# Performance work log

Measured on AMD Instinct MI355X. Metric: run time of the kernel, lower is better.

## Reference

```python
import jax, jax.numpy as jnp
import numpy as np
import math

EMBED = 256
HEADS = 4
HEAD_DIM = EMBED // HEADS
OUT_DIM = 256
LN_EPS = 1e-5


def _qkv_init(key):
    # diagonal-domination init from Galerkin Transformer (Cao): U(-spread,spread)*gain + delta*I
    spread = math.sqrt(3.0 / EMBED)
    gain, delta = 0.01, 0.01
    w = jax.random.uniform(key, (EMBED, EMBED), minval=-spread, maxval=spread) * gain
    return w + delta * jnp.eye(EMBED, dtype=w.dtype)


def setup_inputs() -> dict:
    key = jax.random.key(0)
    ks = jax.random.split(key, 6)
    seq = jax.random.normal(ks[0], (4, 8192, EMBED), dtype=jnp.float32)
    wq = _qkv_init(ks[1])
    wk = _qkv_init(ks[2])
    wv = _qkv_init(ks[3])
    # nn.Linear default init for wo
    bound = 1.0 / math.sqrt(EMBED)
    wo = jax.random.uniform(ks[4], (OUT_DIM, EMBED), minval=-bound, maxval=bound)
    bo = jax.random.uniform(ks[5], (OUT_DIM,), minval=-bound, maxval=bound)
    ln_k_g = jnp.ones((HEAD_DIM,), jnp.float32)
    ln_k_b = jnp.zeros((HEAD_DIM,), jnp.float32)
    ln_v_g = jnp.ones((HEAD_DIM,), jnp.float32)
    ln_v_b = jnp.zeros((HEAD_DIM,), jnp.float32)
    return {"seq": seq, "wq": wq, "wk": wk, "wv": wv, "wo": wo, "bo": bo,
            "ln_k_g": ln_k_g, "ln_k_b": ln_k_b, "ln_v_g": ln_v_g, "ln_v_b": ln_v_b}


def _layer_norm(x, g, b):
    mu = jnp.mean(x, axis=-1, keepdims=True)
    var = jnp.mean(jnp.square(x - mu), axis=-1, keepdims=True)
    return (x - mu) * jax.lax.rsqrt(var + LN_EPS) * g + b


def _split_heads(x, B, S):
    # [B, S, E] -> [B, H, S, D]
    return x.reshape(B, S, HEADS, HEAD_DIM).transpose(0, 2, 1, 3)


def reference(seq, wq, wk, wv, wo, bo, ln_k_g, ln_k_b, ln_v_g, ln_v_b):
    B, S, _ = seq.shape
    q = _split_heads(seq @ wq.T, B, S)
    k = _split_heads(seq @ wk.T, B, S)
    v = _split_heads(seq @ wv.T, B, S)
    k = _layer_norm(k, ln_k_g, ln_k_b)
    v = _layer_norm(v, ln_v_g, ln_v_b)
    # Galerkin (softmax-free) attention: Q @ (K^T V) / n  -- O(n d^2)
    kv = jnp.einsum('bhsd,bhse->bhde', k, v) / S   # [B,H,D,D]
    ga = jnp.einsum('bhsd,bhde->bhse', q, kv)       # [B,H,S,D]
    ga = ga.transpose(0, 2, 1, 3).reshape(B, S, EMBED)
    return ga @ wo.T + bo
```

## Files before the change

### kernel.cpp

```cpp
#include <hip/hip_runtime.h>
#include <hip/hip_bf16.h>
#include <stdint.h>


#define EMBED 256
#define SEQ   8192
#define LN_EPS 1e-5f

using bf16x8 = __attribute__((ext_vector_type(8))) short;
using bf16x4 = __attribute__((ext_vector_type(4))) short;
using f32x4  = __attribute__((ext_vector_type(4))) float;

static __device__ __forceinline__ short f2bf(float f) {
  __hip_bfloat16 h = __float2bfloat16(f);
  return __builtin_bit_cast(short, h);
}
static __device__ __forceinline__ float bf2f(uint32_t u) {
  return __uint_as_float(u << 16);
}

#define MFMA16(a, b, c) __builtin_amdgcn_mfma_f32_16x16x32_bf16((a), (b), (c), 0, 0, 0)

template <int ROWS>
static __device__ __forceinline__ void stage_x(char* smem, const float* __restrict__ src, int tid) {
#pragma unroll
  for (int i = 0; i < ROWS / 8; ++i) {
    int g = tid + i * 256;
    int row = g >> 5, c16 = g & 31;
    const f32x4* p = (const f32x4*)(src + row * EMBED + c16 * 8);
    f32x4 f0 = p[0], f1 = p[1];
    bf16x8 v;
    v[0] = f2bf(f0[0]); v[1] = f2bf(f0[1]); v[2] = f2bf(f0[2]); v[3] = f2bf(f0[3]);
    v[4] = f2bf(f1[0]); v[5] = f2bf(f1[1]); v[6] = f2bf(f1[2]); v[7] = f2bf(f1[3]);
    *(bf16x8*)(smem + row * 512 + ((c16 * 16) ^ ((row & 7) << 4))) = v;
  }
}

__global__ void gka_prep(const float* __restrict__ wq, const float* __restrict__ wk,
                         const float* __restrict__ wv,
                         unsigned short* __restrict__ wkf, unsigned short* __restrict__ wvf,
                         unsigned short* __restrict__ wqt) {
  __shared__ unsigned short T[64 * 66];
  int blk = blockIdx.x, tid = threadIdx.x;
  if (blk < 64) {
    int g = (blk & 31) * 256 + tid;
    const float* W = (blk < 32) ? wk : wv;
    unsigned short* D = (blk < 32) ? wkf : wvf;
    int wid = g >> 11, kk = (g >> 8) & 7, n = (g >> 6) & 3, ln = g & 63;
    int row = wid * 64 + n * 16 + (ln & 15);
    int c0 = kk * 32 + (ln >> 4) * 8;
    const f32x4* p = (const f32x4*)(W + row * 256 + c0);
    f32x4 f0 = p[0], f1 = p[1];
    bf16x8 v;
    v[0] = f2bf(f0[0]); v[1] = f2bf(f0[1]); v[2] = f2bf(f0[2]); v[3] = f2bf(f0[3]);
    v[4] = f2bf(f1[0]); v[5] = f2bf(f1[1]); v[6] = f2bf(f1[2]); v[7] = f2bf(f1[3]);
    *(bf16x8*)(D + g * 8) = v;
    return;
  }
  int t = blk - 64, ti = t >> 2, tj = t & 3;
#pragma unroll
  for (int it = 0; it < 4; ++it) {
    int g = tid + it * 256;
    int jl = g >> 4, g4 = g & 15;
    f32x4 f = *(const f32x4*)(wq + (tj * 64 + jl) * 256 + ti * 64 + g4 * 4);
#pragma unroll
    for (int q = 0; q < 4; ++q) T[jl * 66 + g4 * 4 + q] = (unsigned short)f2bf(f[q]);
  }
  __syncthreads();
#pragma unroll
  for (int it = 0; it < 2; ++it) {
    int g = tid + it * 256;
    int il = g >> 3, j8 = g & 7;
    bf16x8 v;
#pragma unroll
    for (int q = 0; q < 8; ++q) v[q] = (short)T[(j8 * 8 + q) * 66 + il];
    *(bf16x8*)(wqt + (ti * 64 + il) * 256 + tj * 64 + j8 * 8) = v;
  }
}

__global__ __launch_bounds__(256, 2)
void gka_kv(const float* __restrict__ seq,
            const unsigned short* __restrict__ wkf, const unsigned short* __restrict__ wvf,
            const float* __restrict__ lkg, const float* __restrict__ lkb,
            const float* __restrict__ lvg, const float* __restrict__ lvb,
            unsigned short* __restrict__ P) {
  __shared__ char smem[65536];
  const int tid = threadIdx.x;
  const int lane = tid & 63;
  const int wid = tid >> 6;
  const int l15 = lane & 15, l4 = lane >> 4, l7 = lane & 7;
  const int tile = blockIdx.x;
  const int b = tile >> 7;
  const int ptile = tile & 127;

  stage_x<64>(smem, seq + (size_t)(b * SEQ + ptile * 64) * EMBED, tid);
  __syncthreads();

  f32x4 acck[4][4], accv[4][4];
#pragma unroll
  for (int m = 0; m < 4; ++m)
#pragma unroll
    for (int n = 0; n < 4; ++n) { acck[m][n] = (f32x4)0.0f; accv[m][n] = (f32x4)0.0f; }

#pragma unroll
  for (int kk = 0; kk < 8; ++kk) {
    bf16x8 af[4], bwk[4], bwv[4];
#pragma unroll
    for (int m = 0; m < 4; ++m) {
      int row = m * 16 + l15;
      af[m] = *(const bf16x8*)(smem + row * 512 + ((kk * 64 + l4 * 16) ^ (l7 << 4)));
    }
#pragma unroll
    for (int n = 0; n < 4; ++n) {
      size_t off = (((wid * 8 + kk) * 4 + n) * 64 + lane) << 3;
      bwk[n] = *(const bf16x8*)(wkf + off);
      bwv[n] = *(const bf16x8*)(wvf + off);
    }
#pragma unroll
    for (int m = 0; m < 4; ++m)
#pragma unroll
      for (int n = 0; n < 4; ++n) {
        acck[m][n] = MFMA16(af[m], bwk[n], acck[m][n]);
        accv[m][n] = MFMA16(af[m], bwv[n], accv[m][n]);
      }
  }

  __syncthreads();

#pragma unroll
  for (int mat = 0; mat < 2; ++mat) {
    const f32x4 (*acc)[4] = mat ? accv : acck;
    const float* gp = mat ? lvg : lkg;
    const float* bp = mat ? lvb : lkb;
    float gv[4], bv[4];
#pragma unroll
    for (int n = 0; n < 4; ++n) { gv[n] = gp[n * 16 + l15]; bv[n] = bp[n * 16 + l15]; }
    char* T = smem + (mat ? 0 : 32768) + wid * 8192;
#pragma unroll
    for (int m = 0; m < 4; ++m) {
      float mu[4], rs[4];
#pragma unroll
      for (int r = 0; r < 4; ++r) {
        float s1 = 0.f, s2 = 0.f;
#pragma unroll
        for (int n = 0; n < 4; ++n) { float x = acc[m][n][r]; s1 += x; s2 += x * x; }
#pragma unroll
        for (int msk = 1; msk < 16; msk <<= 1) {
          s1 += __shfl_xor(s1, msk);
          s2 += __shfl_xor(s2, msk);
        }
        mu[r] = s1 * (1.f / 64.f);
        float var = s2 * (1.f / 64.f) - mu[r] * mu[r];
        rs[r] = rsqrtf(var + LN_EPS);
      }
#pragma unroll
      for (int n = 0; n < 4; ++n) {
        bf16x4 pk;
#pragma unroll
        for (int r = 0; r < 4; ++r)
          pk[r] = f2bf((acc[m][n][r] - mu[r]) * rs[r] * gv[n] + bv[n]);
        int d = n * 16 + l15;
        int sb = m * 32 + l4 * 8;
        *(bf16x4*)(T + d * 128 + (sb ^ (l7 << 4))) = pk;
      }
    }
  }

  __syncthreads();

  f32x4 a2[4][4];
#pragma unroll
  for (int fd = 0; fd < 4; ++fd)
#pragma unroll
    for (int n = 0; n < 4; ++n) a2[fd][n] = (f32x4)0.0f;

#pragma unroll
  for (int kk = 0; kk < 2; ++kk) {
    bf16x8 ak[4], bv2[4];
#pragma unroll
    for (int fd = 0; fd < 4; ++fd) {
      int d = fd * 16 + l15;
      ak[fd] = *(const bf16x8*)(smem + 32768 + wid * 8192 + d * 128 +
                                ((kk * 64 + l4 * 16) ^ (l7 << 4)));
    }
#pragma unroll
    for (int n = 0; n < 4; ++n) {
      int e = n * 16 + l15;
      bv2[n] = *(const bf16x8*)(smem + wid * 8192 + e * 128 +
                                ((kk * 64 + l4 * 16) ^ (l7 << 4)));
    }
#pragma unroll
    for (int fd = 0; fd < 4; ++fd)
#pragma unroll
      for (int n = 0; n < 4; ++n)
        a2[fd][n] = MFMA16(ak[fd], bv2[n], a2[fd][n]);
  }

  unsigned short* Ph = P + ((size_t)((b * 128 + ptile) * 4 + wid) << 12);
#pragma unroll
  for (int fd = 0; fd < 4; ++fd)
#pragma unroll
    for (int n = 0; n < 4; ++n) {
      bf16x4 pk;
#pragma unroll
      for (int r = 0; r < 4; ++r) pk[r] = f2bf(a2[fd][n][r]);
      *(bf16x4*)(Ph + (fd * 4 + n) * 256 + lane * 4) = pk;
    }
}

__global__ __launch_bounds__(256)
void gka_red(const unsigned short* __restrict__ P, float* __restrict__ kvf) {
  int gtid = blockIdx.x * 256 + threadIdx.x;
  int chunk = gtid & 7;
  int qid = gtid >> 3;
  int b = qid >> 12, h = (qid >> 10) & 3, t4 = qid & 1023;
  const unsigned short* p0 = P + ((size_t)(b * 512 + h) << 12) + t4 * 4;
  float s0 = 0.f, s1 = 0.f, s2 = 0.f, s3 = 0.f;
#pragma unroll
  for (int s = 0; s < 16; ++s) {
    int p = chunk * 16 + s;
    uint2 u = *(const uint2*)(p0 + ((size_t)p << 14));
    s0 += bf2f(u.x & 0xffffu); s1 += bf2f(u.x >> 16);
    s2 += bf2f(u.y & 0xffffu); s3 += bf2f(u.y >> 16);
  }
#pragma unroll
  for (int msk = 1; msk < 8; msk <<= 1) {
    s0 += __shfl_xor(s0, msk); s1 += __shfl_xor(s1, msk);
    s2 += __shfl_xor(s2, msk); s3 += __shfl_xor(s3, msk);
  }
  if (chunk == 0) {
    f32x4 r; r[0] = s0; r[1] = s1; r[2] = s2; r[3] = s3;
    *(f32x4*)(kvf + (qid << 2)) = r;
  }
}

__global__ __launch_bounds__(256, 2)
void gka_m1(const float* __restrict__ kvf, const float* __restrict__ wo,
            unsigned short* __restrict__ m1t) {
  const int tid = threadIdx.x;
  const int lane = tid & 63;
  const int wid = tid >> 6;
  const int l15 = lane & 15, l4 = lane >> 4;
  const int blk = blockIdx.x;
  const int b = blk >> 2, h = blk & 3;
  const float invS = 1.f / (float)SEQ;
  const float* kvh = kvf + ((b * 4 + h) << 12);

  f32x4 acc[4][4];
#pragma unroll
  for (int m = 0; m < 4; ++m)
#pragma unroll
    for (int n = 0; n < 4; ++n) acc[m][n] = (f32x4)0.0f;

#pragma unroll
  for (int kk = 0; kk < 2; ++kk) {
    bf16x8 af[4], bw[4];
#pragma unroll
    for (int m = 0; m < 4; ++m) {
      int base = (m * 4 + kk * 2 + (l4 >> 1)) * 256 +
                 ((l15 >> 2) * 16 + (l4 & 1) * 8) * 4 + (l15 & 3);
      bf16x8 v;
#pragma unroll
      for (int j = 0; j < 8; ++j) v[j] = f2bf(kvh[base + j * 4] * invS);
      af[m] = v;
    }
#pragma unroll
    for (int n = 0; n < 4; ++n) {
      int o = wid * 64 + n * 16 + l15;
      const f32x4* wp = (const f32x4*)(wo + (size_t)o * 256 + h * 64 + kk * 32 + l4 * 8);
      f32x4 w0 = wp[0], w1 = wp[1];
      bf16x8 v;
      v[0] = f2bf(w0[0]); v[1] = f2bf(w0[1]); v[2] = f2bf(w0[2]); v[3] = f2bf(w0[3]);
      v[4] = f2bf(w1[0]); v[5] = f2bf(w1[1]); v[6] = f2bf(w1[2]); v[7] = f2bf(w1[3]);
      bw[n] = v;
    }
#pragma unroll
    for (int m = 0; m < 4; ++m)
#pragma unroll
      for (int n = 0; n < 4; ++n)
        acc[m][n] = MFMA16(af[m], bw[n], acc[m][n]);
  }
#pragma unroll
  for (int m = 0; m < 4; ++m)
#pragma unroll
    for (int n = 0; n < 4; ++n) {
      int o = wid * 64 + n * 16 + l15;
      int j0 = h * 64 + m * 16 + l4 * 4;
      bf16x4 pk;
#pragma unroll
      for (int r = 0; r < 4; ++r) pk[r] = f2bf(acc[m][n][r]);
      *(bf16x4*)(m1t + (size_t)(b * 256 + o) * 256 + j0) = pk;
    }
}

__global__ __launch_bounds__(512, 2)
void gka_wc(const unsigned short* __restrict__ wqt, const unsigned short* __restrict__ m1t,
            unsigned short* __restrict__ wcf) {
  const int tid = threadIdx.x;
  const int lane = tid & 63;
  const int wid = tid >> 6;
  const int wm = wid >> 2, wn = wid & 3;
  const int l15 = lane & 15, l4 = lane >> 4;
  const int blk = blockIdx.x;
  const int b = blk >> 1, ih = blk & 1;

  f32x4 acc[4][4];
#pragma unroll
  for (int m = 0; m < 4; ++m)
#pragma unroll
    for (int n = 0; n < 4; ++n) acc[m][n] = (f32x4)0.0f;

#pragma unroll
  for (int kk = 0; kk < 8; ++kk) {
    bf16x8 af[4], bw[4];
#pragma unroll
    for (int m = 0; m < 4; ++m) {
      int i = ih * 128 + wm * 64 + m * 16 + l15;
      af[m] = *(const bf16x8*)(wqt + i * 256 + kk * 32 + l4 * 8);
    }
#pragma unroll
    for (int n = 0; n < 4; ++n) {
      int o = wn * 64 + n * 16 + l15;
      bw[n] = *(const bf16x8*)(m1t + (size_t)(b * 256 + o) * 256 + kk * 32 + l4 * 8);
    }
#pragma unroll
    for (int m = 0; m < 4; ++m)
#pragma unroll
      for (int n = 0; n < 4; ++n)
        acc[m][n] = MFMA16(af[m], bw[n], acc[m][n]);
  }
#pragma unroll
  for (int m = 0; m < 4; ++m)
#pragma unroll
    for (int n = 0; n < 4; ++n) {
      int kko = ih * 4 + wm * 2 + (m >> 1);
      int laneo = ((m & 1) * 2 + (l4 >> 1)) * 16 + l15;
      int jo = (l4 & 1) * 4;
      bf16x4 pk;
#pragma unroll
      for (int r = 0; r < 4; ++r) pk[r] = f2bf(acc[m][n][r]);
      *(bf16x4*)(wcf + ((size_t)b << 16) +
                 (((((wn * 8 + kko) * 4 + n) * 64) + laneo) << 3) + jo) = pk;
    }
}

__global__ __launch_bounds__(256, 4)
void gka_out(const float* __restrict__ seq, const unsigned short* __restrict__ wcf,
             const float* __restrict__ bo, float* __restrict__ out) {
  __shared__ char smem[16384];
  const int tid = threadIdx.x;
  const int lane = tid & 63;
  const int wid = tid >> 6;
  const int l15 = lane & 15, l4 = lane >> 4, l7 = lane & 7;
  const int tile = blockIdx.x;
  const int b = tile >> 8;
  const int srow = (tile & 255) * 32;

  stage_x<32>(smem, seq + (size_t)(b * SEQ + srow) * EMBED, tid);

  const unsigned short* Wf = wcf + ((size_t)b << 16);
  float bov[4];
#pragma unroll
  for (int n = 0; n < 4; ++n) bov[n] = bo[wid * 64 + n * 16 + l15];

  f32x4 acc[2][4];
#pragma unroll
  for (int m = 0; m < 2; ++m)
#pragma unroll
    for (int n = 0; n < 4; ++n) acc[m][n] = (f32x4)0.0f;

  __syncthreads();

#pragma unroll
  for (int kk = 0; kk < 8; ++kk) {
    bf16x8 af[2], bw[4];
#pragma unroll
    for (int m = 0; m < 2; ++m) {
      int row = m * 16 + l15;
      af[m] = *(const bf16x8*)(smem + row * 512 + ((kk * 64 + l4 * 16) ^ (l7 << 4)));
    }
#pragma unroll
    for (int n = 0; n < 4; ++n)
      bw[n] = *(const bf16x8*)(Wf + ((((wid * 8 + kk) * 4 + n) * 64 + lane) << 3));
#pragma unroll
    for (int m = 0; m < 2; ++m)
#pragma unroll
      for (int n = 0; n < 4; ++n)
        acc[m][n] = MFMA16(af[m], bw[n], acc[m][n]);
  }

  float* dst = out + (size_t)(b * SEQ + srow) * EMBED;
#pragma unroll
  for (int m = 0; m < 2; ++m)
#pragma unroll
    for (int n = 0; n < 4; ++n)
#pragma unroll
      for (int r = 0; r < 4; ++r)
        dst[(size_t)(m * 16 + l4 * 4 + r) * EMBED + wid * 64 + n * 16 + l15] =
            acc[m][n][r] + bov[n];
}

extern "C" void kernel_launch(void* const* d_in, const int* in_sizes, int n_in,
                              void* d_out, int out_size, void* d_ws, size_t ws_size,
                              hipStream_t stream) {
  const float* seq = (const float*)d_in[0];
  const float* wq  = (const float*)d_in[1];
  const float* wk  = (const float*)d_in[2];
  const float* wv  = (const float*)d_in[3];
  const float* wo  = (const float*)d_in[4];
  const float* bo  = (const float*)d_in[5];
  const float* lkg = (const float*)d_in[6];
  const float* lkb = (const float*)d_in[7];
  const float* lvg = (const float*)d_in[8];
  const float* lvb = (const float*)d_in[9];
  float* out = (float*)d_out;
  char* ws = (char*)d_ws;

  unsigned short* wkf = (unsigned short*)(ws + 0);
  unsigned short* wvf = (unsigned short*)(ws + 131072);
  unsigned short* wqt = (unsigned short*)(ws + 262144);
  float*          kvf = (float*)(ws + 524288);
  unsigned short* m1t = (unsigned short*)(ws + 786432);
  unsigned short* wcf = (unsigned short*)(ws + 1310720);
  unsigned short* P   = (unsigned short*)d_out;

  gka_prep<<<80, 256, 0, stream>>>(wq, wk, wv, wkf, wvf, wqt);
  gka_kv<<<512, 256, 0, stream>>>(seq, wkf, wvf, lkg, lkb, lvg, lvb, P);
  gka_red<<<512, 256, 0, stream>>>(P, kvf);
  gka_m1<<<16, 256, 0, stream>>>(kvf, wo, m1t);
  gka_wc<<<8, 512, 0, stream>>>(wqt, m1t, wcf);
  gka_out<<<1024, 256, 0, stream>>>(seq, wcf, bo, out);
}
```

Baseline: 73.50 us.

## Fuse m1 and wc kernels, staging M1 in swizzled shared memory

Merges the kernel computing M1 = (kv/S)·Wo into the kernel computing the combined weight Wc. Each block now computes a half of M1 for one batch into 64KB of XOR-swizzled LDS, synchronises, then multiplies Wq^T by it. This removes one kernel launch and the global round trip of m1t. In exchange only 8 blocks do all of the m1 work, versus 16 blocks before, and 64KB of LDS per block limits occupancy.

```diff
diff --git a/kernel.cpp b/kernel.cpp
--- a/kernel.cpp
+++ b/kernel.cpp
@@ -234,114 +234,113 @@
   }
 }
 
-__global__ __launch_bounds__(256, 2)
-void gka_m1(const float* __restrict__ kvf, const float* __restrict__ wo,
-            unsigned short* __restrict__ m1t) {
+__global__ __launch_bounds__(512)
+void gka_wc(const float* __restrict__ kvf, const float* __restrict__ wo,
+            const unsigned short* __restrict__ wqt, unsigned short* __restrict__ wcf) {
+  __shared__ char M1[65536];
   const int tid = threadIdx.x;
   const int lane = tid & 63;
   const int wid = tid >> 6;
   const int l15 = lane & 15, l4 = lane >> 4;
   const int blk = blockIdx.x;
-  const int b = blk >> 2, h = blk & 3;
+  const int b = blk >> 1, oh = blk & 1;
   const float invS = 1.f / (float)SEQ;
-  const float* kvh = kvf + ((b * 4 + h) << 12);
-
-  f32x4 acc[4][4];
-#pragma unroll
-  for (int m = 0; m < 4; ++m)
-#pragma unroll
-    for (int n = 0; n < 4; ++n) acc[m][n] = (f32x4)0.0f;
-
-#pragma unroll
-  for (int kk = 0; kk < 2; ++kk) {
-    bf16x8 af[4], bw[4];
-#pragma unroll
-    for (int m = 0; m < 4; ++m) {
-      int base = (m * 4 + kk * 2 + (l4 >> 1)) * 256 +
-                 ((l15 >> 2) * 16 + (l4 & 1) * 8) * 4 + (l15 & 3);
-      bf16x8 v;
-#pragma unroll
-      for (int j = 0; j < 8; ++j) v[j] = f2bf(kvh[base + j * 4] * invS);
-      af[m] = v;
-    }
-#pragma unroll
-    for (int n = 0; n < 4; ++n) {
-      int o = wid * 64 + n * 16 + l15;
-      const f32x4* wp = (const f32x4*)(wo + (size_t)o * 256 + h * 64 + kk * 32 + l4 * 8);
-      f32x4 w0 = wp[0], w1 = wp[1];
-      bf16x8 v;
-      v[0] = f2bf(w0[0]); v[1] = f2bf(w0[1]); v[2] = f2bf(w0[2]); v[3] = f2bf(w0[3]);
-      v[4] = f2bf(w1[0]); v[5] = f2bf(w1[1]); v[6] = f2bf(w1[2]); v[7] = f2bf(w1[3]);
-      bw[n] = v;
-    }
+
+  {
+    const int wo_t = wid >> 2, wj = wid & 3;
+    const float* kvh = kvf + ((b * 4 + wj) << 12);
+    f32x4 acc[4][4];
 #pragma unroll
     for (int m = 0; m < 4; ++m)
 #pragma unroll
-      for (int n = 0; n < 4; ++n)
-        acc[m][n] = MFMA16(af[m], bw[n], acc[m][n]);
-  }
-#pragma unroll
-  for (int m = 0; m < 4; ++m)
-#pragma unroll
-    for (int n = 0; n < 4; ++n) {
-      int o = wid * 64 + n * 16 + l15;
-      int j0 = h * 64 + m * 16 + l4 * 4;
-      bf16x4 pk;
-#pragma unroll
-      for (int r = 0; r < 4; ++r) pk[r] = f2bf(acc[m][n][r]);
-      *(bf16x4*)(m1t + (size_t)(b * 256 + o) * 256 + j0) = pk;
-    }
-}
-
-__global__ __launch_bounds__(512, 2)
-void gka_wc(const unsigned short* __restrict__ wqt, const unsigned short* __restrict__ m1t,
-            unsigned short* __restrict__ wcf) {
-  const int tid = threadIdx.x;
-  const int lane = tid & 63;
-  const int wid = tid >> 6;
-  const int wm = wid >> 2, wn = wid & 3;
-  const int l15 = lane & 15, l4 = lane >> 4;
-  const int blk = blockIdx.x;
-  const int b = blk >> 1, ih = blk & 1;
-
-  f32x4 acc[4][4];
-#pragma unroll
-  for (int m = 0; m < 4; ++m)
-#pragma unroll
-    for (int n = 0; n < 4; ++n) acc[m][n] = (f32x4)0.0f;
-
-#pragma unroll
-  for (int kk = 0; kk < 8; ++kk) {
-    bf16x8 af[4], bw[4];
-#pragma unroll
-    for (int m = 0; m < 4; ++m) {
-      int i = ih * 128 + wm * 64 + m * 16 + l15;
-      af[m] = *(const bf16x8*)(wqt + i * 256 + kk * 32 + l4 * 8);
-    }
-#pragma unroll
-    for (int n = 0; n < 4; ++n) {
-      int o = wn * 64 + n * 16 + l15;
-      bw[n] = *(const bf16x8*)(m1t + (size_t)(b * 256 + o) * 256 + kk * 32 + l4 * 8);
+      for (int n = 0; n < 4; ++n) acc[m][n] = (f32x4)0.0f;
+
+#pragma unroll
+    for (int kk = 0; kk < 2; ++kk) {
+      bf16x8 af[4], bw[4];
+#pragma unroll
+      for (int m = 0; m < 4; ++m) {
+        int base = (m * 4 + kk * 2 + (l4 >> 1)) * 256 +
+                   ((l15 >> 2) * 16 + (l4 & 1) * 8) * 4 + (l15 & 3);
+        bf16x8 v;
+#pragma unroll
+        for (int j = 0; j < 8; ++j) v[j] = f2bf(kvh[base + j * 4] * invS);
+        af[m] = v;
+      }
+#pragma unroll
+      for (int n = 0; n < 4; ++n) {
+        int o = oh * 128 + wo_t * 64 + n * 16 + l15;
+        const f32x4* wp = (const f32x4*)(wo + (size_t)o * 256 + wj * 64 + kk * 32 + l4 * 8);
+        f32x4 w0 = wp[0], w1 = wp[1];
+        bf16x8 v;
+        v[0] = f2bf(w0[0]); v[1] = f2bf(w0[1]); v[2] = f2bf(w0[2]); v[3] = f2bf(w0[3]);
+        v[4] = f2bf(w1[0]); v[5] = f2bf(w1[1]); v[6] = f2bf(w1[2]); v[7] = f2bf(w1[3]);
+        bw[n] = v;
+      }
+#pragma unroll
+      for (int m = 0; m < 4; ++m)
+#pragma unroll
+        for (int n = 0; n < 4; ++n)
+          acc[m][n] = MFMA16(af[m], bw[n], acc[m][n]);
     }
 #pragma unroll
     for (int m = 0; m < 4; ++m)
 #pragma unroll
-      for (int n = 0; n < 4; ++n)
-        acc[m][n] = MFMA16(af[m], bw[n], acc[m][n]);
-  }
-#pragma unroll
-  for (int m = 0; m < 4; ++m)
-#pragma unroll
-    for (int n = 0; n < 4; ++n) {
-      int kko = ih * 4 + wm * 2 + (m >> 1);
-      int laneo = ((m & 1) * 2 + (l4 >> 1)) * 16 + l15;
-      int jo = (l4 & 1) * 4;
-      bf16x4 pk;
-#pragma unroll
-      for (int r = 0; r < 4; ++r) pk[r] = f2bf(acc[m][n][r]);
-      *(bf16x4*)(wcf + ((size_t)b << 16) +
-                 (((((wn * 8 + kko) * 4 + n) * 64) + laneo) << 3) + jo) = pk;
-    }
+      for (int n = 0; n < 4; ++n) {
+        int row = wo_t * 64 + n * 16 + l15;
+        int jb = (wj * 64 + m * 16 + l4 * 4) * 2;
+        bf16x4 pk;
+#pragma unroll
+        for (int r = 0; r < 4; ++r) pk[r] = f2bf(acc[m][n][r]);
+        *(bf16x4*)(M1 + row * 512 + (jb ^ ((row & 7) << 4))) = pk;
+      }
+  }
+
+  __syncthreads();
+
+  {
+    const int wi = wid >> 1, wo2 = wid & 1;
+    f32x4 acc[4][4];
+#pragma unroll
+    for (int m = 0; m < 4; ++m)
+#pragma unroll
+      for (int n = 0; n < 4; ++n) acc[m][n] = (f32x4)0.0f;
+
+#pragma unroll
+    for (int kk = 0; kk < 8; ++kk) {
+      bf16x8 af[4], bw[4];
+#pragma unroll
+      for (int m = 0; m < 4; ++m) {
+        int i = wi * 64 + m * 16 + l15;
+        af[m] = *(const bf16x8*)(wqt + i * 256 + kk * 32 + l4 * 8);
+      }
+#pragma unroll
+      for (int n = 0; n < 4; ++n) {
+        int row = wo2 * 64 + n * 16 + l15;
+        bw[n] = *(const bf16x8*)(M1 + row * 512 +
+                                 ((kk * 64 + l4 * 16) ^ ((row & 7) << 4)));
+      }
+#pragma unroll
+      for (int m = 0; m < 4; ++m)
+#pragma unroll
+        for (int n = 0; n < 4; ++n)
+          acc[m][n] = MFMA16(af[m], bw[n], acc[m][n]);
+    }
+    const int o6 = oh * 2 + wo2;
+#pragma unroll
+    for (int m = 0; m < 4; ++m)
+#pragma unroll
+      for (int n = 0; n < 4; ++n) {
+        int kko = wi * 2 + (m >> 1);
+        int laneo = ((m & 1) * 2 + (l4 >> 1)) * 16 + l15;
+        int jo = (l4 & 1) * 4;
+        bf16x4 pk;
+#pragma unroll
+        for (int r = 0; r < 4; ++r) pk[r] = f2bf(acc[m][n][r]);
+        *(bf16x4*)(wcf + ((size_t)b << 16) +
+                   (((((o6 * 8 + kko) * 4 + n) * 64) + laneo) << 3) + jo) = pk;
+      }
+  }
 }
 
 __global__ __launch_bounds__(256, 4)
@@ -420,14 +419,12 @@
   unsigned short* wvf = (unsigned short*)(ws + 131072);
   unsigned short* wqt = (unsigned short*)(ws + 262144);
   float*          kvf = (float*)(ws + 524288);
-  unsigned short* m1t = (unsigned short*)(ws + 786432);
   unsigned short* wcf = (unsigned short*)(ws + 1310720);
   unsigned short* P   = (unsigned short*)d_out;
 
   gka_prep<<<80, 256, 0, stream>>>(wq, wk, wv, wkf, wvf, wqt);
   gka_kv<<<512, 256, 0, stream>>>(seq, wkf, wvf, lkg, lkb, lvg, lvb, P);
   gka_red<<<512, 256, 0, stream>>>(P, kvf);
-  gka_m1<<<16, 256, 0, stream>>>(kvf, wo, m1t);
-  gka_wc<<<8, 512, 0, stream>>>(wqt, m1t, wcf);
+  gka_wc<<<8, 512, 0, stream>>>(kvf, wo, wqt, wcf);
   gka_out<<<1024, 256, 0, stream>>>(seq, wcf, bo, out);
 }
```

Result: faster. 67.39 us (-8.3%).
